# Performance work log

Measured on AMD Instinct MI355X. Metric: run time of the kernel, lower is better.

The kernel has to match this reference:

```python
import jax, jax.numpy as jnp
import numpy as np

B, TIN, TOUT = 128, 512, 64
IN_F, OUT_F, H = 64, 32, 1024
DEC_IN = IN_F + OUT_F  # decoder GRU input size


def setup_inputs() -> dict:
    key = jax.random.key(0)
    ks = jax.random.split(key, 24)
    s = 1.0 / np.sqrt(H)
    u = lambda k, shp: jax.random.uniform(k, shp, jnp.float32, -s, s)
    return {
        "enc_input": jax.random.normal(ks[0], (B, TIN, IN_F), jnp.float32),
        "dec_input": jax.random.normal(ks[1], (B, TOUT, IN_F), jnp.float32),
        # encoder GRU, layer 0 (input IN_F) and layer 1 (input H); gates stacked [r,z,n]
        "enc_Wih0": u(ks[2], (3 * H, IN_F)), "enc_Whh0": u(ks[3], (3 * H, H)),
        "enc_bih0": u(ks[4], (3 * H,)), "enc_bhh0": u(ks[5], (3 * H,)),
        "enc_Wih1": u(ks[6], (3 * H, H)), "enc_Whh1": u(ks[7], (3 * H, H)),
        "enc_bih1": u(ks[8], (3 * H,)), "enc_bhh1": u(ks[9], (3 * H,)),
        # decoder GRU, layer 0 (input DEC_IN) and layer 1 (input H)
        "dec_Wih0": u(ks[10], (3 * H, DEC_IN)), "dec_Whh0": u(ks[11], (3 * H, H)),
        "dec_bih0": u(ks[12], (3 * H,)), "dec_bhh0": u(ks[13], (3 * H,)),
        "dec_Wih1": u(ks[14], (3 * H, H)), "dec_Whh1": u(ks[15], (3 * H, H)),
        "dec_bih1": u(ks[16], (3 * H,)), "dec_bhh1": u(ks[17], (3 * H,)),
        # output MLP: Linear(H,H)+ReLU, then Linear(H,OUT_F, bias=False)
        "out1_W": u(ks[18], (H, H)), "out1_b": u(ks[19], (H,)),
        "out2_W": u(ks[20], (OUT_F, H)),
    }


def _gru_cell(x, h, Wih, Whh, bih, bhh):
    """Single GRU step, PyTorch gate convention. x:(B,in) h:(B,H) -> (B,H)."""
    gi = x @ Wih.T + bih
    gh = h @ Whh.T + bhh
    ir, iz, inn = jnp.split(gi, 3, axis=-1)
    hr, hz, hn = jnp.split(gh, 3, axis=-1)
    r = jax.nn.sigmoid(ir + hr)
    z = jax.nn.sigmoid(iz + hz)
    n = jnp.tanh(inn + r * hn)
    return (1.0 - z) * n + z * h


def _gru_layer(x, h0, Wih, Whh, bih, bhh):
    """Full-sequence GRU layer. x:(B,T,in) -> (ys:(B,T,H), hT:(B,H))."""
    xp = jnp.einsum('bti,gi->btg', x, Wih) + bih  # precompute input projections
    def step(h, g):
        gh = h @ Whh.T + bhh
        ir, iz, inn = jnp.split(g, 3, axis=-1)
        hr, hz, hn = jnp.split(gh, 3, axis=-1)
        r = jax.nn.sigmoid(ir + hr)
        z = jax.nn.sigmoid(iz + hz)
        n = jnp.tanh(inn + r * hn)
        hnew = (1.0 - z) * n + z * h
        return hnew, hnew
    hT, ys = jax.lax.scan(step, h0, jnp.swapaxes(xp, 0, 1))
    return jnp.swapaxes(ys, 0, 1), hT


def _forward(enc_input, dec_input,
             enc_Wih0, enc_Whh0, enc_bih0, enc_bhh0,
             enc_Wih1, enc_Whh1, enc_bih1, enc_bhh1,
             dec_Wih0, dec_Whh0, dec_bih0, dec_bhh0,
             dec_Wih1, dec_Whh1, dec_bih1, dec_bhh1,
             out1_W, out1_b, out2_W):
    b = enc_input.shape[0]
    zeros = jnp.zeros((b, H), enc_input.dtype)
    # encoder: 2-layer GRU from zero state
    y0, eh0 = _gru_layer(enc_input, zeros, enc_Wih0, enc_Whh0, enc_bih0, enc_bhh0)
    _, eh1 = _gru_layer(y0, zeros, enc_Wih1, enc_Whh1, enc_bih1, enc_bhh1)
    y_prev0 = enc_input[:, -1, :OUT_F]
    def dec_step(carry, x_t):
        y_prev, h0, h1 = carry
        x = jnp.concatenate([y_prev, x_t], axis=-1)  # (B, OUT_F+IN_F)
        h0n = _gru_cell(x, h0, dec_Wih0, dec_Whh0, dec_bih0, dec_bhh0)
        h1n = _gru_cell(h0n, h1, dec_Wih1, dec_Whh1, dec_bih1, dec_bhh1)
        out = jax.nn.relu(h1n @ out1_W.T + out1_b) @ out2_W.T  # dropout=identity (eval)
        return (out, h0n, h1n), out
    _, ys = jax.lax.scan(dec_step, (y_prev0, eh0, eh1), jnp.swapaxes(dec_input, 0, 1))
    return jnp.swapaxes(ys, 0, 1)  # (B, TOUT, OUT_F)


def reference(enc_input, dec_input,
              enc_Wih0, enc_Whh0, enc_bih0, enc_bhh0,
              enc_Wih1, enc_Whh1, enc_bih1, enc_bhh1,
              dec_Wih0, dec_Whh0, dec_bih0, dec_bhh0,
              dec_Wih1, dec_Whh1, dec_bih1, dec_bhh1,
              out1_W, out1_b, out2_W):
    return _forward(enc_input, dec_input,
                    enc_Wih0, enc_Whh0, enc_bih0, enc_bhh0,
                    enc_Wih1, enc_Whh1, enc_bih1, enc_bhh1,
                    dec_Wih0, dec_Whh0, dec_bih0, dec_bhh0,
                    dec_Wih1, dec_Whh1, dec_bih1, dec_bhh1,
                    out1_W, out1_b, out2_W)
```

## Files before the change

### kernel.cpp

```cpp
#include <hip/hip_runtime.h>

typedef unsigned short u16;
typedef __attribute__((ext_vector_type(8))) short bf16x8;
typedef __attribute__((ext_vector_type(4))) float f32x4;

#define Bsz   128
#define TIN   512
#define TOUT  64
#define INF   64
#define OUTF  32
#define Hdim  1024
#define H3    3072

#define K0    1088
#define K1    2048
#define KD0   1120
#define KD1   2048
#define KH    1024

__device__ __forceinline__ u16 f2bf(float f) {
    union { float f; unsigned u; } c; c.f = f;
    unsigned u = c.u;
    unsigned r = (u + 0x7fffu + ((u >> 16) & 1u)) >> 16;
    return (u16)r;
}

__device__ __forceinline__ f32x4 mfma16(bf16x8 a, bf16x8 b, f32x4 c) {
    return __builtin_amdgcn_mfma_f32_16x16x32_bf16(a, b, c, 0, 0, 0);
}


__global__ void __launch_bounds__(256) pack2(
        const float* __restrict__ A, int KA,
        const float* __restrict__ Bs, int KB,
        u16* __restrict__ dst) {
    int row = blockIdx.y;
    int k = blockIdx.x * 256 + threadIdx.x;
    int K = KA + KB;
    if (k >= K) return;
    float v = (k < KA) ? A[(size_t)row * KA + k] : Bs[(size_t)row * KB + (k - KA)];
    dst[(size_t)row * K + k] = f2bf(v);
}

__global__ void __launch_bounds__(256) pack_bias(
        const float* bi0e, const float* bh0e,
        const float* bi1e, const float* bh1e,
        const float* bi0d, const float* bh0d,
        const float* bi1d, const float* bh1d,
        const float* out1b,
        float* B0, float* B1, float* BD0, float* BD1, float* HB) {
    int j = blockIdx.x * blockDim.x + threadIdx.x;
    if (j >= 1024) return;
    const float* bis[4] = { bi0e, bi1e, bi0d, bi1d };
    const float* bhs[4] = { bh0e, bh1e, bh0d, bh1d };
    float* ds[4] = { B0, B1, BD0, BD1 };
#pragma unroll
    for (int s = 0; s < 4; ++s) {
        ds[s][j]        = bis[s][j]        + bhs[s][j];
        ds[s][1024 + j] = bis[s][1024 + j] + bhs[s][1024 + j];
        ds[s][2048 + j] = bis[s][2048 + j];
        ds[s][3072 + j] = bhs[s][2048 + j];
    }
    HB[j] = out1b[j];
}

__global__ void __launch_bounds__(256) init_state(
        const float* __restrict__ enc_input,
        u16* __restrict__ X0, u16* __restrict__ X1,
        float* __restrict__ H0f, float* __restrict__ H1f) {
    int gtid = blockIdx.x * blockDim.x + threadIdx.x;
    int G = gridDim.x * blockDim.x;
    for (int i = gtid; i < Bsz * Hdim; i += G) { int b = i >> 10, j = i & 1023; X0[(size_t)b * K0 + j] = 0; }
    for (int i = gtid; i < Bsz * INF; i += G) { int b = i >> 6, f = i & 63;
        X0[(size_t)b * K0 + 1024 + f] = f2bf(enc_input[(size_t)b * (TIN * INF) + f]); }
    for (int i = gtid; i < Bsz * Hdim; i += G) { int b = i >> 10, j = i & 1023;
        X1[(size_t)(Bsz * K1) + (size_t)b * K1 + 1024 + j] = 0; }
    for (int i = gtid; i < Bsz * Hdim; i += G) { H0f[i] = 0.f; H1f[Bsz * Hdim + i] = 0.f; }
}

template <int H_FIRST>
__device__ __forceinline__ void gru_tile(
    const u16* __restrict__ W, const u16* __restrict__ X,
    const float* __restrict__ Hold, const float* __restrict__ Bias,
    int K, int kbSplit, int kbTotal, int ct, int nb0,
    float* __restrict__ Hnew,
    u16* __restrict__ O1, int ld1, int off1,
    u16* __restrict__ O2, int ld2, int off2) {
    const int tid = threadIdx.x, lane = tid & 63, w = tid >> 6;
    const int l15 = lane & 15, kq = lane >> 4;
    const int j0 = ct * 16;
    const int nb = nb0 + w * 16 + l15;
    const u16* Wr = W + (size_t)(j0 + l15) * K + kq * 8;
    const u16* Wz = Wr + (size_t)1024 * K;
    const u16* Wn = Wz + (size_t)1024 * K;
    const u16* Xb = X + (size_t)nb * K + kq * 8;
    f32x4 accR = {0.f, 0.f, 0.f, 0.f};
    f32x4 accZ = {0.f, 0.f, 0.f, 0.f};
    f32x4 acc2 = {0.f, 0.f, 0.f, 0.f};
    f32x4 acc3 = {0.f, 0.f, 0.f, 0.f};
    for (int kb = 0; kb < kbSplit; ++kb) {
        const int o = kb * 32;
        bf16x8 xb = *(const bf16x8*)(Xb + o);
        accR = mfma16(*(const bf16x8*)(Wr + o), xb, accR);
        accZ = mfma16(*(const bf16x8*)(Wz + o), xb, accZ);
        acc2 = mfma16(*(const bf16x8*)(Wn + o), xb, acc2);
    }
    for (int kb = kbSplit; kb < kbTotal; ++kb) {
        const int o = kb * 32;
        bf16x8 xb = *(const bf16x8*)(Xb + o);
        accR = mfma16(*(const bf16x8*)(Wr + o), xb, accR);
        accZ = mfma16(*(const bf16x8*)(Wz + o), xb, accZ);
        acc3 = mfma16(*(const bf16x8*)(Wn + o), xb, acc3);
    }
    f32x4 accH = H_FIRST ? acc2 : acc3;
    f32x4 accI = H_FIRST ? acc3 : acc2;
#pragma unroll
    for (int q = 0; q < 4; ++q) {
        const int j = j0 + kq * 4 + q;
        float r = 1.f / (1.f + expf(-(accR[q] + Bias[j])));
        float z = 1.f / (1.f + expf(-(accZ[q] + Bias[1024 + j])));
        float n = tanhf(accI[q] + Bias[2048 + j] + r * (accH[q] + Bias[3072 + j]));
        float ho = Hold[(size_t)j * Bsz + nb];
        float hv = (1.f - z) * n + z * ho;
        Hnew[(size_t)j * Bsz + nb] = hv;
        u16 hb = f2bf(hv);
        O1[(size_t)nb * ld1 + off1 + j] = hb;
        if (O2) O2[(size_t)nb * ld2 + off2 + j] = hb;
    }
}

struct KParams {
    const float* enc_input;
    const float* dec_input;
    const u16 *W0, *W1, *WD0, *WD1, *WH1, *WH2;
    const float *B0, *B1, *BD0, *BD1, *HB;
    u16 *X0, *X1, *XD0, *XD1, *Hhead, *Abuf;
    float *H0f, *H1f;
    float* out;
};

#define SX0  (Bsz * K0)
#define SX1  (Bsz * K1)
#define SXD0 (Bsz * KD0)
#define SXD1 (Bsz * KD1)
#define SH   (Bsz * Hdim)

__global__ void __launch_bounds__(256) enc_round(KParams p, int r) {
    const int wg = blockIdx.x;
    const int pr = r & 1, pw = pr ^ 1;
    if (wg < 128) {
        if (r < 512) {
            gru_tile<1>(p.W0, p.X0 + pr * SX0, p.H0f + pr * SH, p.B0,
                        K0, 32, 34, wg >> 1, (wg & 1) * 64,
                        p.H0f + pw * SH,
                        p.X0 + pw * SX0, K0, 0,
                        p.X1 + pw * SX1, K1, 0);
            if (r + 1 < 512 && threadIdx.x < 64) {
                int b = wg, f = threadIdx.x;
                p.X0[(size_t)pw * SX0 + (size_t)b * K0 + 1024 + f] =
                    f2bf(p.enc_input[((size_t)b * TIN + (r + 1)) * INF + f]);
            }
        }
    } else {
        if (r >= 1) {
            int w2 = wg - 128;
            gru_tile<0>(p.W1, p.X1 + pr * SX1, p.H1f + pr * SH, p.B1,
                        K1, 32, 64, w2 >> 1, (w2 & 1) * 64,
                        p.H1f + pw * SH,
                        p.X1 + pw * SX1, K1, 1024,
                        (u16*)nullptr, 0, 0);
        }
    }
}

__global__ void __launch_bounds__(256) transition(KParams p) {
    int gtid = blockIdx.x * 256 + threadIdx.x;
    const int G = 256 * 256;
    float* H1a = p.H1f;
    float* H1b = p.H1f + SH;
    for (int i = gtid; i < SH; i += G) H1a[i] = H1b[i];
    for (int i = gtid; i < Bsz * OUTF; i += G) {
        int b = i >> 5, f = i & 31;
        p.XD0[(size_t)b * KD0 + f] = f2bf(p.enc_input[((size_t)b * TIN + (TIN - 1)) * INF + f]);
    }
    for (int i = gtid; i < Bsz * INF; i += G) {
        int b = i >> 6, f = i & 63;
        p.XD0[(size_t)b * KD0 + 32 + f] = f2bf(p.dec_input[(size_t)b * (TOUT * INF) + f]);
    }
    for (int i = gtid; i < Bsz * Hdim; i += G) {
        int b = i >> 10, j = i & 1023;
        p.XD0[(size_t)b * KD0 + 96 + j] = p.X0[(size_t)b * K0 + j];
    }
    for (int i = gtid; i < Bsz * Hdim; i += G) {
        int b = i >> 10, j = i & 1023;
        p.XD1[(size_t)b * KD1 + 1024 + j] = p.X1[(size_t)SX1 + (size_t)b * K1 + 1024 + j];
    }
}

__global__ void __launch_bounds__(256) dec_A(KParams p, int t) {
    const int wg = blockIdx.x;
    const int pt = t & 1, pn = pt ^ 1;
    gru_tile<0>(p.WD0, p.XD0 + pt * SXD0, p.H0f + pt * SH, p.BD0,
                KD0, 3, 35, wg >> 1, (wg & 1) * 64,
                p.H0f + pn * SH,
                p.XD0 + pn * SXD0, KD0, 96,
                p.XD1 + pt * SXD1, KD1, 0);
}

__global__ void __launch_bounds__(256) dec_B(KParams p, int t) {
    const int wg = blockIdx.x;
    const int pt = t & 1, pn = pt ^ 1;
    gru_tile<0>(p.WD1, p.XD1 + pt * SXD1, p.H1f + pt * SH, p.BD1,
                KD1, 32, 64, wg >> 1, (wg & 1) * 64,
                p.H1f + pn * SH,
                p.XD1 + pn * SXD1, KD1, 1024,
                p.Hhead, KH, 0);
}

__global__ void __launch_bounds__(256) dec_C(KParams p, int t) {
    const int wg = blockIdx.x;
    const int pn = (t & 1) ^ 1;
    const int tid = threadIdx.x, lane = tid & 63, w = tid >> 6;
    const int l15 = lane & 15, kq = lane >> 4;
    const int ct = wg >> 1, nb0 = (wg & 1) * 64;
    const int j0 = ct * 16;
    const int nb = nb0 + w * 16 + l15;
    const u16* Wr = p.WH1 + (size_t)(j0 + l15) * KH + kq * 8;
    const u16* Xb = p.Hhead + (size_t)nb * KH + kq * 8;
    f32x4 acc = {0.f, 0.f, 0.f, 0.f};
    for (int kb = 0; kb < KH / 32; ++kb) {
        const int o = kb * 32;
        acc = mfma16(*(const bf16x8*)(Wr + o), *(const bf16x8*)(Xb + o), acc);
    }
#pragma unroll
    for (int q = 0; q < 4; ++q) {
        const int j = j0 + kq * 4 + q;
        float v = acc[q] + p.HB[j];
        v = v > 0.f ? v : 0.f;
        p.Abuf[(size_t)nb * KH + j] = f2bf(v);
    }
    if (t + 1 < TOUT && wg < 128 && threadIdx.x < 64) {
        int b = wg, f = threadIdx.x;
        p.XD0[(size_t)pn * SXD0 + (size_t)b * KD0 + 32 + f] =
            f2bf(p.dec_input[((size_t)b * TOUT + (t + 1)) * INF + f]);
    }
}

__global__ void __launch_bounds__(256) dec_D(KParams p, int t) {
    __shared__ float sred[1024];
    const int wg = blockIdx.x;
    const int pn = (t & 1) ^ 1;
    const int tid = threadIdx.x, lane = tid & 63, w = tid >> 6;
    const int l15 = lane & 15, kq = lane >> 4;
    const int mt = wg & 1, nt = wg >> 1;
    const u16* Wr = p.WH2 + (size_t)(mt * 16 + l15) * KH + kq * 8;
    const u16* Xb = p.Abuf + (size_t)(nt * 16 + l15) * KH + kq * 8;
    f32x4 acc = {0.f, 0.f, 0.f, 0.f};
    for (int kb = w * 8; kb < w * 8 + 8; ++kb) {
        const int o = kb * 32;
        acc = mfma16(*(const bf16x8*)(Wr + o), *(const bf16x8*)(Xb + o), acc);
    }
#pragma unroll
    for (int q = 0; q < 4; ++q) sred[(w * 64 + lane) * 4 + q] = acc[q];
    __syncthreads();
    if (w == 0) {
#pragma unroll
        for (int q = 0; q < 4; ++q) {
            float s = sred[(0 * 64 + lane) * 4 + q] + sred[(1 * 64 + lane) * 4 + q] +
                      sred[(2 * 64 + lane) * 4 + q] + sred[(3 * 64 + lane) * 4 + q];
            int feat = mt * 16 + kq * 4 + q;
            int b = nt * 16 + l15;
            p.out[(size_t)b * (TOUT * OUTF) + t * OUTF + feat] = s;
            p.XD0[(size_t)pn * SXD0 + (size_t)b * KD0 + feat] = f2bf(s);
        }
    }
}

extern "C" void kernel_launch(void* const* d_in, const int* in_sizes, int n_in,
                              void* d_out, int out_size, void* d_ws, size_t ws_size,
                              hipStream_t stream) {
    const float* enc_input = (const float*)d_in[0];
    const float* dec_input = (const float*)d_in[1];
    const float* enc_Wih0 = (const float*)d_in[2];
    const float* enc_Whh0 = (const float*)d_in[3];
    const float* enc_bih0 = (const float*)d_in[4];
    const float* enc_bhh0 = (const float*)d_in[5];
    const float* enc_Wih1 = (const float*)d_in[6];
    const float* enc_Whh1 = (const float*)d_in[7];
    const float* enc_bih1 = (const float*)d_in[8];
    const float* enc_bhh1 = (const float*)d_in[9];
    const float* dec_Wih0 = (const float*)d_in[10];
    const float* dec_Whh0 = (const float*)d_in[11];
    const float* dec_bih0 = (const float*)d_in[12];
    const float* dec_bhh0 = (const float*)d_in[13];
    const float* dec_Wih1 = (const float*)d_in[14];
    const float* dec_Whh1 = (const float*)d_in[15];
    const float* dec_bih1 = (const float*)d_in[16];
    const float* dec_bhh1 = (const float*)d_in[17];
    const float* out1_W = (const float*)d_in[18];
    const float* out1_b = (const float*)d_in[19];
    const float* out2_W = (const float*)d_in[20];

    char* ws = (char*)d_ws;
    size_t off = 0;
    auto alloc = [&](size_t bytes) { size_t o = off; off = (off + bytes + 255) & ~(size_t)255; return o; };

    u16* W0 = (u16*)(ws + alloc((size_t)H3 * K0 * 2));
    u16* W1 = (u16*)(ws + alloc((size_t)H3 * K1 * 2));
    u16* WD0 = (u16*)(ws + alloc((size_t)H3 * KD0 * 2));
    u16* WD1 = (u16*)(ws + alloc((size_t)H3 * KD1 * 2));
    u16* WH1 = (u16*)(ws + alloc((size_t)Hdim * KH * 2));
    u16* WH2 = (u16*)(ws + alloc((size_t)OUTF * KH * 2));
    float* B0 = (float*)(ws + alloc(4096 * 4));
    float* B1 = (float*)(ws + alloc(4096 * 4));
    float* BD0 = (float*)(ws + alloc(4096 * 4));
    float* BD1 = (float*)(ws + alloc(4096 * 4));
    float* HB = (float*)(ws + alloc(1024 * 4));
    u16* X0 = (u16*)(ws + alloc((size_t)2 * Bsz * K0 * 2));
    u16* X1 = (u16*)(ws + alloc((size_t)2 * Bsz * K1 * 2));
    u16* XD0 = (u16*)(ws + alloc((size_t)2 * Bsz * KD0 * 2));
    u16* XD1 = (u16*)(ws + alloc((size_t)2 * Bsz * KD1 * 2));
    float* H0f = (float*)(ws + alloc((size_t)2 * Bsz * Hdim * 4));
    float* H1f = (float*)(ws + alloc((size_t)2 * Bsz * Hdim * 4));
    u16* Hhead = (u16*)(ws + alloc((size_t)Bsz * KH * 2));
    u16* Abuf = (u16*)(ws + alloc((size_t)Bsz * KH * 2));

    pack2<<<dim3((K0 + 255) / 256, H3), 256, 0, stream>>>(enc_Whh0, 1024, enc_Wih0, 64, W0);
    pack2<<<dim3((K1 + 255) / 256, H3), 256, 0, stream>>>(enc_Wih1, 1024, enc_Whh1, 1024, W1);
    pack2<<<dim3((KD0 + 255) / 256, H3), 256, 0, stream>>>(dec_Wih0, 96, dec_Whh0, 1024, WD0);
    pack2<<<dim3((KD1 + 255) / 256, H3), 256, 0, stream>>>(dec_Wih1, 1024, dec_Whh1, 1024, WD1);
    pack2<<<dim3((KH + 255) / 256, Hdim), 256, 0, stream>>>(out1_W, 1024, nullptr, 0, WH1);
    pack2<<<dim3((KH + 255) / 256, OUTF), 256, 0, stream>>>(out2_W, 1024, nullptr, 0, WH2);
    pack_bias<<<4, 256, 0, stream>>>(enc_bih0, enc_bhh0, enc_bih1, enc_bhh1,
                                     dec_bih0, dec_bhh0, dec_bih1, dec_bhh1,
                                     out1_b, B0, B1, BD0, BD1, HB);
    init_state<<<256, 256, 0, stream>>>(enc_input, X0, X1, H0f, H1f);

    KParams kp;
    kp.enc_input = enc_input; kp.dec_input = dec_input;
    kp.W0 = W0; kp.W1 = W1; kp.WD0 = WD0; kp.WD1 = WD1; kp.WH1 = WH1; kp.WH2 = WH2;
    kp.B0 = B0; kp.B1 = B1; kp.BD0 = BD0; kp.BD1 = BD1; kp.HB = HB;
    kp.X0 = X0; kp.X1 = X1; kp.XD0 = XD0; kp.XD1 = XD1; kp.Hhead = Hhead; kp.Abuf = Abuf;
    kp.H0f = H0f; kp.H1f = H1f;
    kp.out = (float*)d_out;

    for (int r = 0; r < 513; ++r)
        enc_round<<<256, 256, 0, stream>>>(kp, r);

    transition<<<256, 256, 0, stream>>>(kp);

    for (int t = 0; t < TOUT; ++t) {
        dec_A<<<128, 256, 0, stream>>>(kp, t);
        dec_B<<<128, 256, 0, stream>>>(kp, t);
        dec_C<<<128, 256, 0, stream>>>(kp, t);
        dec_D<<<16, 256, 0, stream>>>(kp, t);
    }
}
```

Measured before the change: 20.11 ms.

## Split GRU K-reduction across two wave groups per block with LDS reduction

Each GRU block now launches 512 threads, and two groups of four waves each cover half of the K range. The partial accumulators are summed through shared memory before the gate math. The weight and input layouts are reordered so the hidden-state part always comes first, which keeps the split between the hidden and input n-gate contributions consistent. The aim is to double the waves available to hide memory latency on the latency-bound recurrent steps, at the cost of one barrier and LDS traffic per step. The MFMA loops are also unrolled.

```diff
diff --git a/kernel.cpp b/kernel.cpp
--- a/kernel.cpp
+++ b/kernel.cpp
@@ -17,6 +17,12 @@
 #define KD0   1120
 #define KD1   2048
 #define KH    1024
+
+#define SX0  (Bsz * K0)
+#define SX1  (Bsz * K1)
+#define SXD0 (Bsz * KD0)
+#define SXD1 (Bsz * KD1)
+#define SH   (Bsz * Hdim)
 
 __device__ __forceinline__ u16 f2bf(float f) {
     union { float f; unsigned u; } c; c.f = f;
@@ -74,58 +80,95 @@
     for (int i = gtid; i < Bsz * INF; i += G) { int b = i >> 6, f = i & 63;
         X0[(size_t)b * K0 + 1024 + f] = f2bf(enc_input[(size_t)b * (TIN * INF) + f]); }
     for (int i = gtid; i < Bsz * Hdim; i += G) { int b = i >> 10, j = i & 1023;
-        X1[(size_t)(Bsz * K1) + (size_t)b * K1 + 1024 + j] = 0; }
-    for (int i = gtid; i < Bsz * Hdim; i += G) { H0f[i] = 0.f; H1f[Bsz * Hdim + i] = 0.f; }
-}
-
-template <int H_FIRST>
-__device__ __forceinline__ void gru_tile(
-    const u16* __restrict__ W, const u16* __restrict__ X,
-    const float* __restrict__ Hold, const float* __restrict__ Bias,
-    int K, int kbSplit, int kbTotal, int ct, int nb0,
-    float* __restrict__ Hnew,
-    u16* __restrict__ O1, int ld1, int off1,
-    u16* __restrict__ O2, int ld2, int off2) {
-    const int tid = threadIdx.x, lane = tid & 63, w = tid >> 6;
+        X1[(size_t)SX1 + (size_t)b * K1 + j] = 0; }
+    for (int i = gtid; i < Bsz * Hdim; i += G) { H0f[i] = 0.f; H1f[SH + i] = 0.f; }
+}
+
+template <int KB0, int KB1, int SPLIT>
+__device__ __forceinline__ void gru_wave(
+        const u16* __restrict__ W, const u16* __restrict__ X, int K,
+        int j0, int nb0w,
+        f32x4& accR, f32x4& accZ, f32x4& accN0, f32x4& accN1) {
+    const int lane = threadIdx.x & 63;
     const int l15 = lane & 15, kq = lane >> 4;
-    const int j0 = ct * 16;
-    const int nb = nb0 + w * 16 + l15;
     const u16* Wr = W + (size_t)(j0 + l15) * K + kq * 8;
     const u16* Wz = Wr + (size_t)1024 * K;
     const u16* Wn = Wz + (size_t)1024 * K;
-    const u16* Xb = X + (size_t)nb * K + kq * 8;
-    f32x4 accR = {0.f, 0.f, 0.f, 0.f};
-    f32x4 accZ = {0.f, 0.f, 0.f, 0.f};
-    f32x4 acc2 = {0.f, 0.f, 0.f, 0.f};
-    f32x4 acc3 = {0.f, 0.f, 0.f, 0.f};
-    for (int kb = 0; kb < kbSplit; ++kb) {
+    const u16* Xb = X + (size_t)(nb0w + l15) * K + kq * 8;
+    accR = (f32x4){0.f, 0.f, 0.f, 0.f};
+    accZ = (f32x4){0.f, 0.f, 0.f, 0.f};
+    accN0 = (f32x4){0.f, 0.f, 0.f, 0.f};
+    accN1 = (f32x4){0.f, 0.f, 0.f, 0.f};
+    constexpr int E0 = (SPLIT < KB1) ? SPLIT : KB1;
+    constexpr int S1 = (SPLIT > KB0) ? SPLIT : KB0;
+#pragma unroll 8
+    for (int kb = KB0; kb < E0; ++kb) {
         const int o = kb * 32;
         bf16x8 xb = *(const bf16x8*)(Xb + o);
-        accR = mfma16(*(const bf16x8*)(Wr + o), xb, accR);
-        accZ = mfma16(*(const bf16x8*)(Wz + o), xb, accZ);
-        acc2 = mfma16(*(const bf16x8*)(Wn + o), xb, acc2);
-    }
-    for (int kb = kbSplit; kb < kbTotal; ++kb) {
+        accR  = mfma16(*(const bf16x8*)(Wr + o), xb, accR);
+        accZ  = mfma16(*(const bf16x8*)(Wz + o), xb, accZ);
+        accN0 = mfma16(*(const bf16x8*)(Wn + o), xb, accN0);
+    }
+#pragma unroll 8
+    for (int kb = S1; kb < KB1; ++kb) {
         const int o = kb * 32;
         bf16x8 xb = *(const bf16x8*)(Xb + o);
-        accR = mfma16(*(const bf16x8*)(Wr + o), xb, accR);
-        accZ = mfma16(*(const bf16x8*)(Wz + o), xb, accZ);
-        acc3 = mfma16(*(const bf16x8*)(Wn + o), xb, acc3);
-    }
-    f32x4 accH = H_FIRST ? acc2 : acc3;
-    f32x4 accI = H_FIRST ? acc3 : acc2;
-#pragma unroll
-    for (int q = 0; q < 4; ++q) {
-        const int j = j0 + kq * 4 + q;
-        float r = 1.f / (1.f + expf(-(accR[q] + Bias[j])));
-        float z = 1.f / (1.f + expf(-(accZ[q] + Bias[1024 + j])));
-        float n = tanhf(accI[q] + Bias[2048 + j] + r * (accH[q] + Bias[3072 + j]));
-        float ho = Hold[(size_t)j * Bsz + nb];
-        float hv = (1.f - z) * n + z * ho;
-        Hnew[(size_t)j * Bsz + nb] = hv;
-        u16 hb = f2bf(hv);
-        O1[(size_t)nb * ld1 + off1 + j] = hb;
-        if (O2) O2[(size_t)nb * ld2 + off2 + j] = hb;
+        accR  = mfma16(*(const bf16x8*)(Wr + o), xb, accR);
+        accZ  = mfma16(*(const bf16x8*)(Wz + o), xb, accZ);
+        accN1 = mfma16(*(const bf16x8*)(Wn + o), xb, accN1);
+    }
+}
+
+template <int KBT, int SPLIT>
+__device__ __forceinline__ void gru_block(
+        const u16* __restrict__ W, const u16* __restrict__ X,
+        const float* __restrict__ Hold, const float* __restrict__ Bias,
+        int K, int ct, int nb0,
+        float* __restrict__ Hnew,
+        u16* __restrict__ O1, int ld1, int off1,
+        u16* __restrict__ O2, int ld2, int off2,
+        float* __restrict__ sred ) {
+    const int tid = threadIdx.x, lane = tid & 63, w = tid >> 6;
+    const int bg = w & 3, grp = w >> 2;
+    const int l15 = lane & 15, kq = lane >> 4;
+    const int j0 = ct * 16;
+    const int nb0w = nb0 + bg * 16;
+    constexpr int MID = KBT / 2;
+
+    f32x4 aR, aZ, aN0, aN1;
+    if (grp == 0) gru_wave<0, MID, SPLIT>(W, X, K, j0, nb0w, aR, aZ, aN0, aN1);
+    else          gru_wave<MID, KBT, SPLIT>(W, X, K, j0, nb0w, aR, aZ, aN0, aN1);
+
+    float* slot = sred + ((size_t)bg * 64 + lane) * 17;
+    if (grp == 1) {
+#pragma unroll
+        for (int q = 0; q < 4; ++q) {
+            slot[q]      = aR[q];
+            slot[4 + q]  = aZ[q];
+            slot[8 + q]  = aN0[q];
+            slot[12 + q] = aN1[q];
+        }
+    }
+    __syncthreads();
+    if (grp == 0) {
+#pragma unroll
+        for (int q = 0; q < 4; ++q) {
+            const int j = j0 + kq * 4 + q;
+            const int nb = nb0w + l15;
+            float R  = aR[q]  + slot[q];
+            float Z  = aZ[q]  + slot[4 + q];
+            float Nh = aN0[q] + slot[8 + q];
+            float Ni = aN1[q] + slot[12 + q];
+            float r = 1.f / (1.f + expf(-(R + Bias[j])));
+            float z = 1.f / (1.f + expf(-(Z + Bias[1024 + j])));
+            float n = tanhf(Ni + Bias[2048 + j] + r * (Nh + Bias[3072 + j]));
+            float ho = Hold[(size_t)j * Bsz + nb];
+            float hv = (1.f - z) * n + z * ho;
+            Hnew[(size_t)j * Bsz + nb] = hv;
+            u16 hb = f2bf(hv);
+            O1[(size_t)nb * ld1 + off1 + j] = hb;
+            if (O2) O2[(size_t)nb * ld2 + off2 + j] = hb;
+        }
     }
 }
 
@@ -139,22 +182,17 @@
     float* out;
 };
 
-#define SX0  (Bsz * K0)
-#define SX1  (Bsz * K1)
-#define SXD0 (Bsz * KD0)
-#define SXD1 (Bsz * KD1)
-#define SH   (Bsz * Hdim)
-
-__global__ void __launch_bounds__(256) enc_round(KParams p, int r) {
+__global__ void __launch_bounds__(512, 2) enc_round(KParams p, int r) {
+    __shared__ float sred[4 * 64 * 17];
     const int wg = blockIdx.x;
     const int pr = r & 1, pw = pr ^ 1;
     if (wg < 128) {
         if (r < 512) {
-            gru_tile<1>(p.W0, p.X0 + pr * SX0, p.H0f + pr * SH, p.B0,
-                        K0, 32, 34, wg >> 1, (wg & 1) * 64,
-                        p.H0f + pw * SH,
-                        p.X0 + pw * SX0, K0, 0,
-                        p.X1 + pw * SX1, K1, 0);
+            gru_block<34, 32>(p.W0, p.X0 + pr * SX0, p.H0f + pr * SH, p.B0,
+                              K0, wg >> 1, (wg & 1) * 64,
+                              p.H0f + pw * SH,
+                              p.X0 + pw * SX0, K0, 0,
+                              p.X1 + pw * SX1, K1, 1024, sred);
             if (r + 1 < 512 && threadIdx.x < 64) {
                 int b = wg, f = threadIdx.x;
                 p.X0[(size_t)pw * SX0 + (size_t)b * K0 + 1024 + f] =
@@ -164,11 +202,11 @@
     } else {
         if (r >= 1) {
             int w2 = wg - 128;
-            gru_tile<0>(p.W1, p.X1 + pr * SX1, p.H1f + pr * SH, p.B1,
-                        K1, 32, 64, w2 >> 1, (w2 & 1) * 64,
-                        p.H1f + pw * SH,
-                        p.X1 + pw * SX1, K1, 1024,
-                        (u16*)nullptr, 0, 0);
+            gru_block<64, 32>(p.W1, p.X1 + pr * SX1, p.H1f + pr * SH, p.B1,
+                              K1, w2 >> 1, (w2 & 1) * 64,
+                              p.H1f + pw * SH,
+                              p.X1 + pw * SX1, K1, 0,
+                              (u16*)nullptr, 0, 0, sred);
         }
     }
 }
@@ -176,45 +214,45 @@
 __global__ void __launch_bounds__(256) transition(KParams p) {
     int gtid = blockIdx.x * 256 + threadIdx.x;
     const int G = 256 * 256;
-    float* H1a = p.H1f;
-    float* H1b = p.H1f + SH;
-    for (int i = gtid; i < SH; i += G) H1a[i] = H1b[i];
+    for (int i = gtid; i < SH; i += G) p.H1f[i] = p.H1f[SH + i];
+    for (int i = gtid; i < Bsz * Hdim; i += G) {
+        int b = i >> 10, j = i & 1023;
+        p.XD0[(size_t)b * KD0 + j] = p.X0[(size_t)b * K0 + j];
+    }
     for (int i = gtid; i < Bsz * OUTF; i += G) {
         int b = i >> 5, f = i & 31;
-        p.XD0[(size_t)b * KD0 + f] = f2bf(p.enc_input[((size_t)b * TIN + (TIN - 1)) * INF + f]);
+        p.XD0[(size_t)b * KD0 + 1024 + f] = f2bf(p.enc_input[((size_t)b * TIN + (TIN - 1)) * INF + f]);
     }
     for (int i = gtid; i < Bsz * INF; i += G) {
         int b = i >> 6, f = i & 63;
-        p.XD0[(size_t)b * KD0 + 32 + f] = f2bf(p.dec_input[(size_t)b * (TOUT * INF) + f]);
+        p.XD0[(size_t)b * KD0 + 1056 + f] = f2bf(p.dec_input[(size_t)b * (TOUT * INF) + f]);
     }
     for (int i = gtid; i < Bsz * Hdim; i += G) {
         int b = i >> 10, j = i & 1023;
-        p.XD0[(size_t)b * KD0 + 96 + j] = p.X0[(size_t)b * K0 + j];
-    }
-    for (int i = gtid; i < Bsz * Hdim; i += G) {
-        int b = i >> 10, j = i & 1023;
-        p.XD1[(size_t)b * KD1 + 1024 + j] = p.X1[(size_t)SX1 + (size_t)b * K1 + 1024 + j];
-    }
-}
-
-__global__ void __launch_bounds__(256) dec_A(KParams p, int t) {
+        p.XD1[(size_t)b * KD1 + j] = p.X1[(size_t)SX1 + (size_t)b * K1 + j];
+    }
+}
+
+__global__ void __launch_bounds__(512, 2) dec_A(KParams p, int t) {
+    __shared__ float sred[4 * 64 * 17];
     const int wg = blockIdx.x;
     const int pt = t & 1, pn = pt ^ 1;
-    gru_tile<0>(p.WD0, p.XD0 + pt * SXD0, p.H0f + pt * SH, p.BD0,
-                KD0, 3, 35, wg >> 1, (wg & 1) * 64,
-                p.H0f + pn * SH,
-                p.XD0 + pn * SXD0, KD0, 96,
-                p.XD1 + pt * SXD1, KD1, 0);
-}
-
-__global__ void __launch_bounds__(256) dec_B(KParams p, int t) {
+    gru_block<35, 32>(p.WD0, p.XD0 + pt * SXD0, p.H0f + pt * SH, p.BD0,
+                      KD0, wg >> 1, (wg & 1) * 64,
+                      p.H0f + pn * SH,
+                      p.XD0 + pn * SXD0, KD0, 0,
+                      p.XD1 + pt * SXD1, KD1, 1024, sred);
+}
+
+__global__ void __launch_bounds__(512, 2) dec_B(KParams p, int t) {
+    __shared__ float sred[4 * 64 * 17];
     const int wg = blockIdx.x;
     const int pt = t & 1, pn = pt ^ 1;
-    gru_tile<0>(p.WD1, p.XD1 + pt * SXD1, p.H1f + pt * SH, p.BD1,
-                KD1, 32, 64, wg >> 1, (wg & 1) * 64,
-                p.H1f + pn * SH,
-                p.XD1 + pn * SXD1, KD1, 1024,
-                p.Hhead, KH, 0);
+    gru_block<64, 32>(p.WD1, p.XD1 + pt * SXD1, p.H1f + pt * SH, p.BD1,
+                      KD1, wg >> 1, (wg & 1) * 64,
+                      p.H1f + pn * SH,
+                      p.XD1 + pn * SXD1, KD1, 0,
+                      p.Hhead, KH, 0, sred);
 }
 
 __global__ void __launch_bounds__(256) dec_C(KParams p, int t) {
@@ -228,6 +266,7 @@
     const u16* Wr = p.WH1 + (size_t)(j0 + l15) * KH + kq * 8;
     const u16* Xb = p.Hhead + (size_t)nb * KH + kq * 8;
     f32x4 acc = {0.f, 0.f, 0.f, 0.f};
+#pragma unroll 8
     for (int kb = 0; kb < KH / 32; ++kb) {
         const int o = kb * 32;
         acc = mfma16(*(const bf16x8*)(Wr + o), *(const bf16x8*)(Xb + o), acc);
@@ -239,9 +278,9 @@
         v = v > 0.f ? v : 0.f;
         p.Abuf[(size_t)nb * KH + j] = f2bf(v);
     }
-    if (t + 1 < TOUT && wg < 128 && threadIdx.x < 64) {
+    if (t + 1 < TOUT && threadIdx.x < 64) {
         int b = wg, f = threadIdx.x;
-        p.XD0[(size_t)pn * SXD0 + (size_t)b * KD0 + 32 + f] =
+        p.XD0[(size_t)pn * SXD0 + (size_t)b * KD0 + 1056 + f] =
             f2bf(p.dec_input[((size_t)b * TOUT + (t + 1)) * INF + f]);
     }
 }
@@ -256,6 +295,7 @@
     const u16* Wr = p.WH2 + (size_t)(mt * 16 + l15) * KH + kq * 8;
     const u16* Xb = p.Abuf + (size_t)(nt * 16 + l15) * KH + kq * 8;
     f32x4 acc = {0.f, 0.f, 0.f, 0.f};
+#pragma unroll 8
     for (int kb = w * 8; kb < w * 8 + 8; ++kb) {
         const int o = kb * 32;
         acc = mfma16(*(const bf16x8*)(Wr + o), *(const bf16x8*)(Xb + o), acc);
@@ -271,7 +311,7 @@
             int feat = mt * 16 + kq * 4 + q;
             int b = nt * 16 + l15;
             p.out[(size_t)b * (TOUT * OUTF) + t * OUTF + feat] = s;
-            p.XD0[(size_t)pn * SXD0 + (size_t)b * KD0 + feat] = f2bf(s);
+            p.XD0[(size_t)pn * SXD0 + (size_t)b * KD0 + 1024 + feat] = f2bf(s);
         }
     }
 }
@@ -326,9 +366,9 @@
     u16* Abuf = (u16*)(ws + alloc((size_t)Bsz * KH * 2));
 
     pack2<<<dim3((K0 + 255) / 256, H3), 256, 0, stream>>>(enc_Whh0, 1024, enc_Wih0, 64, W0);
-    pack2<<<dim3((K1 + 255) / 256, H3), 256, 0, stream>>>(enc_Wih1, 1024, enc_Whh1, 1024, W1);
-    pack2<<<dim3((KD0 + 255) / 256, H3), 256, 0, stream>>>(dec_Wih0, 96, dec_Whh0, 1024, WD0);
-    pack2<<<dim3((KD1 + 255) / 256, H3), 256, 0, stream>>>(dec_Wih1, 1024, dec_Whh1, 1024, WD1);
+    pack2<<<dim3((K1 + 255) / 256, H3), 256, 0, stream>>>(enc_Whh1, 1024, enc_Wih1, 1024, W1);
+    pack2<<<dim3((KD0 + 255) / 256, H3), 256, 0, stream>>>(dec_Whh0, 1024, dec_Wih0, 96, WD0);
+    pack2<<<dim3((KD1 + 255) / 256, H3), 256, 0, stream>>>(dec_Whh1, 1024, dec_Wih1, 1024, WD1);
     pack2<<<dim3((KH + 255) / 256, Hdim), 256, 0, stream>>>(out1_W, 1024, nullptr, 0, WH1);
     pack2<<<dim3((KH + 255) / 256, OUTF), 256, 0, stream>>>(out2_W, 1024, nullptr, 0, WH2);
     pack_bias<<<4, 256, 0, stream>>>(enc_bih0, enc_bhh0, enc_bih1, enc_bhh1,
@@ -345,13 +385,13 @@
     kp.out = (float*)d_out;
 
     for (int r = 0; r < 513; ++r)
-        enc_round<<<256, 256, 0, stream>>>(kp, r);
+        enc_round<<<256, 512, 0, stream>>>(kp, r);
 
     transition<<<256, 256, 0, stream>>>(kp);
 
     for (int t = 0; t < TOUT; ++t) {
-        dec_A<<<128, 256, 0, stream>>>(kp, t);
-        dec_B<<<128, 256, 0, stream>>>(kp, t);
+        dec_A<<<128, 512, 0, stream>>>(kp, t);
+        dec_B<<<128, 512, 0, stream>>>(kp, t);
         dec_C<<<128, 256, 0, stream>>>(kp, t);
         dec_D<<<16, 256, 0, stream>>>(kp, t);
     }
```

Result: slower. 20.66 ms (+2.7%).
